# Performance work log

Hardware: AMD Instinct MI355X
Metric: run time of the kernel (lower is better)

## Reference

```python
import jax, jax.numpy as jnp
import numpy as np

D_MODEL = 512
NUM_HEADS = 8
D_K = D_MODEL // NUM_HEADS


def setup_inputs() -> dict:
    key = jax.random.key(0)
    ks = jax.random.split(key, 10)
    B, L, D = 2, 4096, D_MODEL
    s = 1.0 / np.sqrt(D)
    x = jax.random.normal(ks[0], (B, L, D), dtype=jnp.float32)
    mask = jax.random.randint(ks[1], (B, L), 0, 2, dtype=jnp.int32)
    Wq = jax.random.normal(ks[2], (D, D), dtype=jnp.float32) * s
    bq = jnp.zeros((D,), dtype=jnp.float32)
    Wk = jax.random.normal(ks[3], (D, D), dtype=jnp.float32) * s
    bk = jnp.zeros((D,), dtype=jnp.float32)
    Wv = jax.random.normal(ks[4], (D, D), dtype=jnp.float32) * s
    bv = jnp.zeros((D,), dtype=jnp.float32)
    Wo = jax.random.normal(ks[5], (D, D), dtype=jnp.float32) * s
    bo = jnp.zeros((D,), dtype=jnp.float32)
    return {"x": x, "mask": mask, "Wq": Wq, "bq": bq, "Wk": Wk, "bk": bk,
            "Wv": Wv, "bv": bv, "Wo": Wo, "bo": bo}


def reference(x, mask, Wq, bq, Wk, bk, Wv, bv, Wo, bo):
    B, L, D = x.shape
    H, dk = NUM_HEADS, D_K
    scale = jnp.sqrt(jnp.asarray(dk, dtype=x.dtype))

    def proj(W, b):
        # (B,L,D) @ (D,D) -> (B,H,L,dk)
        return (x @ W.T + b).reshape(B, L, H, dk).transpose(0, 2, 1, 3)

    Q = proj(Wq, bq)
    K = proj(Wk, bk)
    V = proj(Wv, bv)
    scores = jnp.einsum('bhqd,bhkd->bhqk', Q, K) / scale
    # padding mask: (B,L) -> (B,1,1,L); masked positions set to -10000
    m = (mask == 0)[:, None, None, :]
    scores = jnp.where(m, jnp.asarray(-10000.0, dtype=scores.dtype), scores)
    attn = jax.nn.softmax(scores, axis=-1)  # dropout is identity in eval mode
    out = jnp.einsum('bhqk,bhkd->bhqd', attn, V)
    out = out.transpose(0, 2, 1, 3).reshape(B, L, D)
    return out @ Wo.T + bo
```

## Files before the change

kernel.cpp:

```cpp
#include <hip/hip_runtime.h>


#define B_  2
#define L_  4096
#define D_  512
#define H_  8
#define BH_ 16
#define M_  8192

typedef __attribute__((ext_vector_type(8)))  short short8;
typedef __attribute__((ext_vector_type(4)))  float f32x4;
typedef __attribute__((ext_vector_type(16))) float f32x16;
typedef unsigned short u16;

#if __has_builtin(__builtin_amdgcn_exp2f)
#define EX2(x) __builtin_amdgcn_exp2f(x)
#else
#define EX2(x) exp2f(x)
#endif

static __device__ __forceinline__ u16 f2b(float f) {
    union { float f; unsigned i; } x; x.f = f;
    unsigned r = x.i + 0x7fff + ((x.i >> 16) & 1);
    return (u16)(r >> 16);
}

static __device__ __forceinline__ unsigned cvt_pk_bf16(float lo, float hi) {
    unsigned r;
    asm("v_cvt_pk_bf16_f32 %0, %1, %2" : "=v"(r) : "v"(lo), "v"(hi));
    return r;
}

static __device__ __forceinline__ uint4 pk8(const float4& a, const float4& b) {
    uint4 o;
    o.x = cvt_pk_bf16(a.x, a.y);
    o.y = cvt_pk_bf16(a.z, a.w);
    o.z = cvt_pk_bf16(b.x, b.y);
    o.w = cvt_pk_bf16(b.z, b.w);
    return o;
}

static __device__ __forceinline__ void stage8f(u16* dst, const float* s) {
    const float4 a = *(const float4*)s;
    const float4 b = *(const float4*)(s + 4);
    *(uint4*)dst = pk8(a, b);
}

static __device__ __forceinline__ short8 mk8(unsigned a, unsigned b,
                                             unsigned c, unsigned d) {
    union { unsigned u[4]; short8 s; } x;
    x.u[0] = a; x.u[1] = b; x.u[2] = c; x.u[3] = d;
    return x.s;
}

__global__ __launch_bounds__(256) void kvproj_kernel(
    const float* __restrict__ x,
    const float* __restrict__ Wk, const float* __restrict__ bk,
    const float* __restrict__ Wv, const float* __restrict__ bv,
    u16* __restrict__ Kws, u16* __restrict__ Vws, int bh0)
{
    __shared__ __align__(16) unsigned char sm[15360];
    u16 (*As)[40]  = (u16(*)[40])sm;
    u16 (*Bks)[40] = (u16(*)[40])(sm + 5120);
    u16 (*Bvs)[40] = (u16(*)[40])(sm + 10240);
    u16 (*Ts)[73]  = (u16(*)[73])sm;

    const int t    = threadIdx.x;
    const int wid  = t >> 6, lane = t & 63;
    const int m15  = lane & 15, quad = lane >> 4;
    const int wm   = wid >> 1, wn = wid & 1;

    const int bh = bh0 + blockIdx.x;
    const int b  = bh >> 3, h = bh & 7;
    const int l0 = blockIdx.y * 64;

    const int lrow = t >> 2;
    const int lcol = (t & 3) * 8;

    const float* Ap  = x  + ((size_t)b * L_ + l0 + lrow) * 512 + lcol;
    const float* Bkp = Wk + (size_t)(h * 64 + lrow) * 512 + lcol;
    const float* Bvp = Wv + (size_t)(h * 64 + lrow) * 512 + lcol;
    float4 a0  = *(const float4*)Ap,  a1  = *(const float4*)(Ap + 4);
    float4 bk0 = *(const float4*)Bkp, bk1 = *(const float4*)(Bkp + 4);
    float4 bv0 = *(const float4*)Bvp, bv1 = *(const float4*)(Bvp + 4);

    f32x4 kacc[2][2] = {};
    f32x4 vacc[2][2] = {};

    for (int k0 = 0; k0 < 512; k0 += 32) {
        __syncthreads();
        *(uint4*)(&As [lrow][lcol]) = pk8(a0, a1);
        *(uint4*)(&Bks[lrow][lcol]) = pk8(bk0, bk1);
        *(uint4*)(&Bvs[lrow][lcol]) = pk8(bv0, bv1);
        __syncthreads();
        if (k0 + 32 < 512) {
            a0  = *(const float4*)(Ap  + k0 + 32); a1  = *(const float4*)(Ap  + k0 + 36);
            bk0 = *(const float4*)(Bkp + k0 + 32); bk1 = *(const float4*)(Bkp + k0 + 36);
            bv0 = *(const float4*)(Bvp + k0 + 32); bv1 = *(const float4*)(Bvp + k0 + 36);
        }

        short8 afr[2], bkf[2], bvf[2];
#pragma unroll
        for (int mi = 0; mi < 2; ++mi)
            afr[mi] = *(const short8*)(&As[wm * 32 + mi * 16 + m15][quad * 8]);
#pragma unroll
        for (int ni = 0; ni < 2; ++ni) {
            bkf[ni] = *(const short8*)(&Bks[wn * 32 + ni * 16 + m15][quad * 8]);
            bvf[ni] = *(const short8*)(&Bvs[wn * 32 + ni * 16 + m15][quad * 8]);
        }
#pragma unroll
        for (int mi = 0; mi < 2; ++mi)
#pragma unroll
            for (int ni = 0; ni < 2; ++ni) {
                kacc[mi][ni] = __builtin_amdgcn_mfma_f32_16x16x32_bf16(
                    afr[mi], bkf[ni], kacc[mi][ni], 0, 0, 0);
                vacc[mi][ni] = __builtin_amdgcn_mfma_f32_16x16x32_bf16(
                    afr[mi], bvf[ni], vacc[mi][ni], 0, 0, 0);
            }
    }

    {
        u16* out = Kws + (size_t)blockIdx.x * (L_ * 64);
#pragma unroll
        for (int mi = 0; mi < 2; ++mi)
#pragma unroll
            for (int ni = 0; ni < 2; ++ni) {
                const int d  = wn * 32 + ni * 16 + m15;
                const float bv_ = bk[h * 64 + d];
#pragma unroll
                for (int r = 0; r < 4; ++r) {
                    const int l = l0 + wm * 32 + mi * 16 + quad * 4 + r;
                    out[(size_t)l * 64 + d] = f2b(kacc[mi][ni][r] + bv_);
                }
            }
    }
    __syncthreads();
#pragma unroll
    for (int mi = 0; mi < 2; ++mi)
#pragma unroll
        for (int ni = 0; ni < 2; ++ni) {
            const int d  = wn * 32 + ni * 16 + m15;
            const float bv_ = bv[h * 64 + d];
#pragma unroll
            for (int r = 0; r < 4; ++r)
                Ts[wm * 32 + mi * 16 + quad * 4 + r][d] = f2b(vacc[mi][ni][r] + bv_);
        }
    __syncthreads();
    {
        u16* Vt = Vws + (size_t)blockIdx.x * ((size_t)64 * L_);
        const int d  = t >> 2;
        const int ls = (t & 3) * 16;
        u16 pk[16];
#pragma unroll
        for (int j = 0; j < 16; ++j) pk[j] = Ts[ls + j][d];
        u16* dst = Vt + (size_t)d * L_ + l0 + ls;
        *(uint4*)dst       = *(const uint4*)pk;
        *(uint4*)(dst + 8) = *(const uint4*)(pk + 8);
    }
}

__global__ __launch_bounds__(512, 4) void attn_kernel(
    const float* __restrict__ x,
    const float* __restrict__ Wq, const float* __restrict__ bq,
    const u16* __restrict__ Kws, const u16* __restrict__ Vws,
    const int* __restrict__ mask,
    float* __restrict__ O, u16* __restrict__ Obf, int bh0)
{
    __shared__ __align__(16) unsigned char sm[34816];
    u16 (*xs)[40]  = (u16(*)[40])sm;
    u16 (*wqs)[40] = (u16(*)[40])(sm + 10240);
    u16 (*Qs)[72]  = (u16(*)[72])sm;
    u16 (*Ks)[64]  = (u16(*)[64])sm;
    u16 (*Vts)[64] = (u16(*)[64])(sm + 8192);
    float* Msb     = (float*)(sm + 16384);

    const int t    = threadIdx.x;
    const int wid  = t >> 6, lane = t & 63;
    const int m15  = lane & 15, quad = lane >> 4;
    const int l5   = lane & 31, hi = lane >> 5;
    const int hi4  = hi * 4;
    const int x7   = l5 & 7;
    const int qg   = wid & 3;
    const int kb   = wid >> 2;
    float* AlfR    = (float*)(sm + 16640) + wid * 32;

    const int bh = bh0 + blockIdx.y;
    const int b  = bh >> 3, h = bh & 7;
    const int q0 = blockIdx.x * 128;
    const u16* Kc  = Kws + (size_t)blockIdx.y * (L_ * 64);
    const u16* Vtc = Vws + (size_t)blockIdx.y * ((size_t)64 * L_);

    const int srow  = t >> 3;
    const int scol8 = (t & 7);
    const int sslot = (scol8 ^ (srow & 7)) * 8;

    uint4 kreg = *(const uint4*)(Kc + (size_t)srow * 64 + scol8 * 8);
    uint4 vreg = *(const uint4*)(Vtc + (size_t)srow * L_ + scol8 * 8);
    int   mreg = (t < 64) ? mask[b * L_ + t] : 0;

    f32x4 qacc[4] = {};
    {
        const int xr = t >> 2, xc = (t & 3) * 8;
        const float* xp = x + ((size_t)b * L_ + q0 + xr) * 512 + xc;
        const float* wp = Wq + (size_t)(h * 64 + xr) * 512 + xc;
        float4 xa0 = *(const float4*)xp, xa1 = *(const float4*)(xp + 4);
        float4 wa0 = {}, wa1 = {};
        if (t < 256) { wa0 = *(const float4*)wp; wa1 = *(const float4*)(wp + 4); }
        for (int k0 = 0; k0 < 512; k0 += 32) {
            __syncthreads();
            *(uint4*)(&xs[xr][xc]) = pk8(xa0, xa1);
            if (t < 256) *(uint4*)(&wqs[xr][xc]) = pk8(wa0, wa1);
            __syncthreads();
            if (k0 + 32 < 512) {
                xa0 = *(const float4*)(xp + k0 + 32); xa1 = *(const float4*)(xp + k0 + 36);
                if (t < 256) {
                    wa0 = *(const float4*)(wp + k0 + 32); wa1 = *(const float4*)(wp + k0 + 36);
                }
            }
            const short8 afr = *(const short8*)(&xs[wid * 16 + m15][quad * 8]);
#pragma unroll
            for (int ni = 0; ni < 4; ++ni) {
                const short8 bfr = *(const short8*)(&wqs[ni * 16 + m15][quad * 8]);
                qacc[ni] = __builtin_amdgcn_mfma_f32_16x16x32_bf16(afr, bfr, qacc[ni], 0, 0, 0);
            }
        }
    }

    const float QSCALE = 0.125f * 1.44269504089f;
    __syncthreads();
#pragma unroll
    for (int ni = 0; ni < 4; ++ni) {
        const float bv_ = bq[h * 64 + ni * 16 + m15];
#pragma unroll
        for (int r = 0; r < 4; ++r)
            Qs[wid * 16 + quad * 4 + r][ni * 16 + m15] =
                f2b((qacc[ni][r] + bv_) * QSCALE);
    }
    __syncthreads();
    short8 qfr[4];
#pragma unroll
    for (int kd = 0; kd < 4; ++kd)
        qfr[kd] = *(const short8*)(&Qs[32 * qg + l5][16 * kd + 8 * hi]);
    __syncthreads();

    float m_i = -1e30f, l_i = 0.0f;
    f32x16 oacc[2];
#pragma unroll
    for (int db = 0; db < 2; ++db)
#pragma unroll
        for (int e = 0; e < 16; ++e) oacc[db][e] = 0.0f;

    for (int kt = 0; kt < 64; ++kt) {
        __syncthreads();
        *(uint4*)(&Ks [srow][sslot]) = kreg;
        *(uint4*)(&Vts[srow][sslot]) = vreg;
        if (t < 64) Msb[t] = (mreg == 0) ? -14427.0f : 0.0f;
        __syncthreads();
        if (kt + 1 < 64) {
            const int k1 = (kt + 1) * 64;
            kreg = *(const uint4*)(Kc + (size_t)(k1 + srow) * 64 + scol8 * 8);
            vreg = *(const uint4*)(Vtc + (size_t)srow * L_ + k1 + scol8 * 8);
            if (t < 64) mreg = mask[b * L_ + k1 + t];
        }

        f32x16 sa;
#pragma unroll
        for (int p = 0; p < 4; ++p) {
            const f32x4 bb = *(const f32x4*)(&Msb[32 * kb + 8 * p + hi4]);
            sa[4*p+0] = bb[0]; sa[4*p+1] = bb[1]; sa[4*p+2] = bb[2]; sa[4*p+3] = bb[3];
        }
#pragma unroll
        for (int kd = 0; kd < 4; ++kd) {
            const short8 kf = *(const short8*)(
                &Ks[32 * kb + l5][(((2 * kd + hi) ^ x7)) * 8]);
            sa = __builtin_amdgcn_mfma_f32_32x32x16_bf16(kf, qfr[kd], sa, 0, 0, 0);
        }

        float mx = fmaxf(
            fmaxf(fmaxf(fmaxf(sa[0], sa[1]),  fmaxf(sa[2], sa[3])),
                  fmaxf(fmaxf(sa[4], sa[5]),  fmaxf(sa[6], sa[7]))),
            fmaxf(fmaxf(fmaxf(sa[8], sa[9]),  fmaxf(sa[10], sa[11])),
                  fmaxf(fmaxf(sa[12], sa[13]), fmaxf(sa[14], sa[15]))));
        mx = fmaxf(mx, __shfl_xor(mx, 32));

        if (__any(mx > m_i)) {
            const float mnew = fmaxf(m_i, mx);
            const float a = EX2(m_i - mnew);
            m_i = mnew;
            l_i *= a;
            if (hi == 0) AlfR[l5] = a;
#pragma unroll
            for (int p = 0; p < 4; ++p) {
                const f32x4 a4 = *(const f32x4*)(&AlfR[8 * p + hi4]);
#pragma unroll
                for (int i = 0; i < 4; ++i) {
                    oacc[0][4*p+i] *= a4[i];
                    oacc[1][4*p+i] *= a4[i];
                }
            }
        }

        float pv[16];
#pragma unroll
        for (int r = 0; r < 16; ++r) pv[r] = EX2(sa[r] - m_i);
        float ss = ((pv[0]+pv[1]) + (pv[2]+pv[3])) + ((pv[4]+pv[5]) + (pv[6]+pv[7]))
                 + ((pv[8]+pv[9]) + (pv[10]+pv[11])) + ((pv[12]+pv[13]) + (pv[14]+pv[15]));
        ss += __shfl_xor(ss, 32);
        l_i += ss;

        unsigned W[8];
#pragma unroll
        for (int m = 0; m < 8; ++m) W[m] = cvt_pk_bf16(pv[2*m], pv[2*m+1]);

#pragma unroll
        for (int c1 = 0; c1 < 2; ++c1) {
            const unsigned X  = hi ? W[4*c1+0] : W[4*c1+2];
            const unsigned Y  = hi ? W[4*c1+1] : W[4*c1+3];
            const unsigned Xp = __shfl_xor((int)X, 32);
            const unsigned Yp = __shfl_xor((int)Y, 32);
            const unsigned w0 = hi ? Xp : W[4*c1+0];
            const unsigned w1 = hi ? Yp : W[4*c1+1];
            const unsigned w2 = hi ? W[4*c1+2] : Xp;
            const unsigned w3 = hi ? W[4*c1+3] : Yp;
            const short8 af = mk8(w0, w1, w2, w3);
            const int kcg = 2 * kb + c1;
#pragma unroll
            for (int db = 0; db < 2; ++db) {
                const short8 vf = *(const short8*)(
                    &Vts[32 * db + l5][(((2 * kcg + hi) ^ x7)) * 8]);
                oacc[db] = __builtin_amdgcn_mfma_f32_32x32x16_bf16(af, vf, oacc[db], 0, 0, 0);
            }
        }
    }

    float* Op  = (float*)sm;
    float* Mp0 = (float*)(sm + 32768);
    float* Mp1 = Mp0 + 128;
    float* FA  = (float*)(sm + 33792);
    float* FB  = FA + 128;

    __syncthreads();
    if (wid >= 4) {
#pragma unroll
        for (int db = 0; db < 2; ++db) {
            const int d = 32 * db + l5;
#pragma unroll
            for (int p = 0; p < 4; ++p) {
                const int qb   = 32 * qg + 8 * p + hi4;
                const int slot = (qb >> 2) ^ l5;
                f32x4 v;
#pragma unroll
                for (int i = 0; i < 4; ++i) v[i] = oacc[db][4*p+i];
                *(f32x4*)(&Op[d * 128 + slot * 4]) = v;
            }
        }
        if (hi == 0) { Mp0[32 * qg + l5] = m_i; Mp1[32 * qg + l5] = l_i; }
    }
    __syncthreads();
    if (wid < 4) {
        const int q5 = 32 * qg + l5;
        const float mB = Mp0[q5], lB = Mp1[q5];
        const float mS = fmaxf(m_i, mB);
        const float aA = EX2(m_i - mS), aB = EX2(mB - mS);
        const float linv = 1.0f / (l_i * aA + lB * aB);
        if (hi == 0) { FA[q5] = aA * linv; FB[q5] = aB * linv; }
#pragma unroll
        for (int db = 0; db < 2; ++db) {
            const int d = 32 * db + l5;
            const int col = h * 64 + d;
#pragma unroll
            for (int p = 0; p < 4; ++p) {
                const int qb   = 32 * qg + 8 * p + hi4;
                const f32x4 fa = *(const f32x4*)(&FA[qb]);
                const f32x4 fb = *(const f32x4*)(&FB[qb]);
                const int slot = (qb >> 2) ^ l5;
                const f32x4 ob = *(const f32x4*)(&Op[d * 128 + slot * 4]);
#pragma unroll
                for (int i = 0; i < 4; ++i) {
                    const float val = oacc[db][4*p+i] * fa[i] + ob[i] * fb[i];
                    const size_t row = (size_t)b * L_ + q0 + qb + i;
                    if (Obf) Obf[row * 512 + col] = f2b(val);
                    else     O  [row * 512 + col] = val;
                }
            }
        }
    }
}

__global__ __launch_bounds__(256) void outproj_v2_kernel(
    const u16* __restrict__ AO,
    const float* __restrict__ Wo, const float* __restrict__ bo,
    float* __restrict__ out)
{
    __shared__ __align__(16) u16 As[64][40];
    __shared__ __align__(16) u16 Bs[64][40];

    const int t    = threadIdx.x;
    const int wid  = t >> 6, lane = t & 63;
    const int m15  = lane & 15, quad = lane >> 4;
    const int wm   = wid >> 1, wn = wid & 1;
    const int bm   = blockIdx.x * 64;
    const int n0   = blockIdx.y * 64;

    const int lrow = t >> 2;
    const int lcol = (t & 3) * 8;

    const u16*   Ap = AO + (size_t)(bm + lrow) * 512 + lcol;
    const float* Bp = Wo + (size_t)(n0 + lrow) * 512 + lcol;
    uint4  areg = *(const uint4*)Ap;
    float4 b0 = *(const float4*)Bp, b1 = *(const float4*)(Bp + 4);

    f32x4 acc[2][2] = {};

    for (int k0 = 0; k0 < 512; k0 += 32) {
        __syncthreads();
        *(uint4*)(&As[lrow][lcol]) = areg;
        *(uint4*)(&Bs[lrow][lcol]) = pk8(b0, b1);
        __syncthreads();
        if (k0 + 32 < 512) {
            areg = *(const uint4*)(Ap + k0 + 32);
            b0 = *(const float4*)(Bp + k0 + 32); b1 = *(const float4*)(Bp + k0 + 36);
        }

        short8 afr[2], bfr[2];
#pragma unroll
        for (int mi = 0; mi < 2; ++mi)
            afr[mi] = *(const short8*)(&As[wm * 32 + mi * 16 + m15][quad * 8]);
#pragma unroll
        for (int ni = 0; ni < 2; ++ni)
            bfr[ni] = *(const short8*)(&Bs[wn * 32 + ni * 16 + m15][quad * 8]);
#pragma unroll
        for (int mi = 0; mi < 2; ++mi)
#pragma unroll
            for (int ni = 0; ni < 2; ++ni)
                acc[mi][ni] = __builtin_amdgcn_mfma_f32_16x16x32_bf16(
                    afr[mi], bfr[ni], acc[mi][ni], 0, 0, 0);
    }

#pragma unroll
    for (int mi = 0; mi < 2; ++mi)
#pragma unroll
        for (int ni = 0; ni < 2; ++ni) {
            const int col = n0 + wn * 32 + ni * 16 + m15;
            const float bv_ = bo[col];
#pragma unroll
            for (int r = 0; r < 4; ++r) {
                const int row = bm + wm * 32 + mi * 16 + quad * 4 + r;
                out[(size_t)row * 512 + col] = acc[mi][ni][r] + bv_;
            }
        }
}

__global__ __launch_bounds__(256) void outproj_inplace_kernel(
    float* __restrict__ AO,
    const float* __restrict__ Wo, const float* __restrict__ bo)
{
    __shared__ __align__(16) u16 As[32][520];
    __shared__ __align__(16) u16 Ws_[64][40];

    const int t    = threadIdx.x;
    const int wid  = t >> 6, lane = t & 63;
    const int m15  = lane & 15, quad = lane >> 4;
    const int wm   = wid >> 1, wn = wid & 1;
    const int bm   = blockIdx.x * 32;

#pragma unroll
    for (int it = 0; it < 8; ++it) {
        const int idx = t + it * 256;
        const int row = idx >> 6, c8 = (idx & 63) * 8;
        stage8f(&As[row][c8], AO + (size_t)(bm + row) * 512 + c8);
    }
    const int lrow = t >> 2;
    const int lcol = (t & 3) * 8;
    __syncthreads();

    for (int n0 = 0; n0 < 512; n0 += 64) {
        f32x4 acc[2] = {};
        for (int k0 = 0; k0 < 512; k0 += 32) {
            __syncthreads();
            stage8f(&Ws_[lrow][lcol], Wo + (size_t)(n0 + lrow) * 512 + k0 + lcol);
            __syncthreads();
            const short8 afr = *(const short8*)(&As[wm * 16 + m15][k0 + quad * 8]);
#pragma unroll
            for (int ni = 0; ni < 2; ++ni) {
                const short8 bfr = *(const short8*)(&Ws_[wn * 32 + ni * 16 + m15][quad * 8]);
                acc[ni] = __builtin_amdgcn_mfma_f32_16x16x32_bf16(afr, bfr, acc[ni], 0, 0, 0);
            }
        }
#pragma unroll
        for (int ni = 0; ni < 2; ++ni) {
            const int col = n0 + wn * 32 + ni * 16 + m15;
            const float bv_ = bo[col];
#pragma unroll
            for (int r = 0; r < 4; ++r) {
                const int row = bm + wm * 16 + quad * 4 + r;
                AO[(size_t)row * 512 + col] = acc[ni][r] + bv_;
            }
        }
    }
}

extern "C" void kernel_launch(void* const* d_in, const int* in_sizes, int n_in,
                              void* d_out, int out_size, void* d_ws, size_t ws_size,
                              hipStream_t stream) {
    const float* x    = (const float*)d_in[0];
    const int*   mask = (const int*)d_in[1];
    const float* Wq = (const float*)d_in[2]; const float* bq = (const float*)d_in[3];
    const float* Wk = (const float*)d_in[4]; const float* bk = (const float*)d_in[5];
    const float* Wv = (const float*)d_in[6]; const float* bv = (const float*)d_in[7];
    const float* Wo = (const float*)d_in[8]; const float* bo = (const float*)d_in[9];

    float* out = (float*)d_out;
    u16*   ws  = (u16*)d_ws;

    const size_t per_bh   = (size_t)2 * L_ * 64 * 2;
    const size_t kv_bytes = (size_t)BH_ * per_bh;
    const size_t ao_bytes = (size_t)M_ * 512 * 2;

    if (ws_size >= kv_bytes + ao_bytes) {
        u16* Kws  = ws;
        u16* Vws  = Kws + (size_t)BH_ * (L_ * 64);
        u16* AOws = ws + kv_bytes / 2;
        kvproj_kernel<<<dim3(BH_, L_ / 64), 256, 0, stream>>>(
            x, Wk, bk, Wv, bv, Kws, Vws, 0);
        attn_kernel<<<dim3(L_ / 128, BH_), 512, 0, stream>>>(
            x, Wq, bq, Kws, Vws, mask, out, AOws, 0);
        outproj_v2_kernel<<<dim3(M_ / 64, 8), 256, 0, stream>>>(AOws, Wo, bo, out);
    } else {
        int chunk = 16;
        while (chunk > 1 && (size_t)chunk * per_bh > ws_size) chunk >>= 1;
        u16* Kws = ws;
        u16* Vws = Kws + (size_t)chunk * (L_ * 64);
        for (int bh0 = 0; bh0 < BH_; bh0 += chunk) {
            kvproj_kernel<<<dim3(chunk, L_ / 64), 256, 0, stream>>>(
                x, Wk, bk, Wv, bv, Kws, Vws, bh0);
            attn_kernel<<<dim3(L_ / 128, chunk), 512, 0, stream>>>(
                x, Wq, bq, Kws, Vws, mask, out, nullptr, bh0);
        }
        outproj_inplace_kernel<<<dim3(M_ / 32), 256, 0, stream>>>(out, Wo, bo);
    }
}
```

Measured before the change: 237.9 us.

## Process two K/V tiles per barrier pair in attention loop

The attention loop now stages two 64-key K/V tiles and their mask values into shared memory per iteration instead of one, halving the number of loop iterations and __syncthreads pairs. It prefetches two tiles into registers ahead of time and runs the tile computation twice per iteration through a lambda. It also drops the barrier after the Q fragment read, relying on the first loop barrier instead. This costs more registers and more shared memory per block, which may lower occupancy at 512 threads with launch bounds of 4.

```diff
diff --git a/kernel.cpp b/kernel.cpp
--- a/kernel.cpp
+++ b/kernel.cpp
@@ -170,9 +170,6 @@
     u16 (*xs)[40]  = (u16(*)[40])sm;
     u16 (*wqs)[40] = (u16(*)[40])(sm + 10240);
     u16 (*Qs)[72]  = (u16(*)[72])sm;
-    u16 (*Ks)[64]  = (u16(*)[64])sm;
-    u16 (*Vts)[64] = (u16(*)[64])(sm + 8192);
-    float* Msb     = (float*)(sm + 16384);
 
     const int t    = threadIdx.x;
     const int wid  = t >> 6, lane = t & 63;
@@ -182,7 +179,12 @@
     const int x7   = l5 & 7;
     const int qg   = wid & 3;
     const int kb   = wid >> 2;
-    float* AlfR    = (float*)(sm + 16640) + wid * 32;
+    u16*   KsA  = (u16*)sm;
+    u16*   KsB  = (u16*)(sm + 8192);
+    u16*   VtsA = (u16*)(sm + 16384);
+    u16*   VtsB = (u16*)(sm + 24576);
+    float* Msb  = (float*)(sm + 32768);
+    float* AlfR = (float*)(sm + 33280) + wid * 32;
 
     const int bh = bh0 + blockIdx.y;
     const int b  = bh >> 3, h = bh & 7;
@@ -194,9 +196,15 @@
     const int scol8 = (t & 7);
     const int sslot = (scol8 ^ (srow & 7)) * 8;
 
-    uint4 kreg = *(const uint4*)(Kc + (size_t)srow * 64 + scol8 * 8);
-    uint4 vreg = *(const uint4*)(Vtc + (size_t)srow * L_ + scol8 * 8);
-    int   mreg = (t < 64) ? mask[b * L_ + t] : 0;
+    uint4 kregA = *(const uint4*)(Kc + (size_t)srow * 64 + scol8 * 8);
+    uint4 vregA = *(const uint4*)(Vtc + (size_t)srow * L_ + scol8 * 8);
+    uint4 kregB = *(const uint4*)(Kc + (size_t)(64 + srow) * 64 + scol8 * 8);
+    uint4 vregB = *(const uint4*)(Vtc + (size_t)srow * L_ + 64 + scol8 * 8);
+    int mregA = 0, mregB = 0;
+    if (t < 64) {
+        mregA = mask[b * L_ + t];
+        mregB = mask[b * L_ + 64 + t];
+    }
 
     f32x4 qacc[4] = {};
     {
@@ -241,7 +249,6 @@
 #pragma unroll
     for (int kd = 0; kd < 4; ++kd)
         qfr[kd] = *(const short8*)(&Qs[32 * qg + l5][16 * kd + 8 * hi]);
-    __syncthreads();
 
     float m_i = -1e30f, l_i = 0.0f;
     f32x16 oacc[2];
@@ -250,29 +257,17 @@
 #pragma unroll
         for (int e = 0; e < 16; ++e) oacc[db][e] = 0.0f;
 
-    for (int kt = 0; kt < 64; ++kt) {
-        __syncthreads();
-        *(uint4*)(&Ks [srow][sslot]) = kreg;
-        *(uint4*)(&Vts[srow][sslot]) = vreg;
-        if (t < 64) Msb[t] = (mreg == 0) ? -14427.0f : 0.0f;
-        __syncthreads();
-        if (kt + 1 < 64) {
-            const int k1 = (kt + 1) * 64;
-            kreg = *(const uint4*)(Kc + (size_t)(k1 + srow) * 64 + scol8 * 8);
-            vreg = *(const uint4*)(Vtc + (size_t)srow * L_ + k1 + scol8 * 8);
-            if (t < 64) mreg = mask[b * L_ + k1 + t];
-        }
-
+    auto tile_body = [&](const u16* KsC, const u16* VtsC, const float* MsbC) {
         f32x16 sa;
 #pragma unroll
         for (int p = 0; p < 4; ++p) {
-            const f32x4 bb = *(const f32x4*)(&Msb[32 * kb + 8 * p + hi4]);
+            const f32x4 bb = *(const f32x4*)(MsbC + 32 * kb + 8 * p + hi4);
             sa[4*p+0] = bb[0]; sa[4*p+1] = bb[1]; sa[4*p+2] = bb[2]; sa[4*p+3] = bb[3];
         }
 #pragma unroll
         for (int kd = 0; kd < 4; ++kd) {
             const short8 kf = *(const short8*)(
-                &Ks[32 * kb + l5][(((2 * kd + hi) ^ x7)) * 8]);
+                KsC + (size_t)(32 * kb + l5) * 64 + (((2 * kd + hi) ^ x7)) * 8);
             sa = __builtin_amdgcn_mfma_f32_32x32x16_bf16(kf, qfr[kd], sa, 0, 0, 0);
         }
 
@@ -327,10 +322,36 @@
 #pragma unroll
             for (int db = 0; db < 2; ++db) {
                 const short8 vf = *(const short8*)(
-                    &Vts[32 * db + l5][(((2 * kcg + hi) ^ x7)) * 8]);
+                    VtsC + (size_t)(32 * db + l5) * 64 + (((2 * kcg + hi) ^ x7)) * 8);
                 oacc[db] = __builtin_amdgcn_mfma_f32_32x32x16_bf16(af, vf, oacc[db], 0, 0, 0);
             }
         }
+    };
+
+    for (int it = 0; it < 32; ++it) {
+        __syncthreads();
+        *(uint4*)(KsA  + srow * 64 + sslot) = kregA;
+        *(uint4*)(VtsA + srow * 64 + sslot) = vregA;
+        *(uint4*)(KsB  + srow * 64 + sslot) = kregB;
+        *(uint4*)(VtsB + srow * 64 + sslot) = vregB;
+        if (t < 64) {
+            Msb[t]      = (mregA == 0) ? -14427.0f : 0.0f;
+            Msb[64 + t] = (mregB == 0) ? -14427.0f : 0.0f;
+        }
+        __syncthreads();
+        if (it + 1 < 32) {
+            const int kA = (2 * it + 2) * 64, kB = kA + 64;
+            kregA = *(const uint4*)(Kc + (size_t)(kA + srow) * 64 + scol8 * 8);
+            vregA = *(const uint4*)(Vtc + (size_t)srow * L_ + kA + scol8 * 8);
+            kregB = *(const uint4*)(Kc + (size_t)(kB + srow) * 64 + scol8 * 8);
+            vregB = *(const uint4*)(Vtc + (size_t)srow * L_ + kB + scol8 * 8);
+            if (t < 64) {
+                mregA = mask[b * L_ + kA + t];
+                mregB = mask[b * L_ + kB + t];
+            }
+        }
+        tile_body(KsA, VtsA, Msb);
+        tile_body(KsB, VtsB, Msb + 64);
     }
 
     float* Op  = (float*)sm;
```

Result: slower. 253.0 us (+6.4%).
